# Optimization experiments

Hardware: AMD Instinct MI355X
Metric: run time of the kernel (lower is better)

Reference implementation:

```python
import jax, jax.numpy as jnp
import numpy as np

K = 7          # kernel_size
PAD = 3        # padding (same-size output)
GROUPS = 8


def _unfold(z, H, W):
    # z: [B, C, H+2p, W+2p] -> patches [B, C, H, W, K*K], flat index = kh*K + kw
    # matches torch .unfold(2,K,1).unfold(3,K,1).view(..., -1)
    return jnp.stack(
        [z[:, :, a:a + H, b:b + W] for a in range(K) for b in range(K)],
        axis=-1,
    )


def setup_inputs() -> dict:
    key = jax.random.key(0)
    ks = jax.random.split(key, 7)
    B, C, H, W = 4, 64, 64, 64
    Cout = 64
    fan_scale = (2.0 / Cout) ** 0.5  # kaiming fan_out, 1x1 conv
    return {
        "x": jax.random.normal(ks[0], (B, C, H, W), jnp.float32),
        "y": jax.random.normal(ks[1], (B, C, H, W), jnp.float32),
        "Wq": jax.random.normal(ks[2], (Cout, C), jnp.float32) * fan_scale,
        "Wk": jax.random.normal(ks[3], (Cout, C), jnp.float32) * fan_scale,
        "Wv": jax.random.normal(ks[4], (Cout, C), jnp.float32) * fan_scale,
        "rel_h": jax.random.normal(ks[5], (Cout // 2, K), jnp.float32),
        "rel_w": jax.random.normal(ks[6], (Cout // 2, K), jnp.float32),
    }


def reference(x, y, Wq, Wk, Wv, rel_h, rel_w):
    B, C, H, W = x.shape
    Cout = Wq.shape[0]
    half = Cout // 2

    # 1x1 convs (no bias) commute with zero padding, so project first.
    q = jnp.einsum('oc,bchw->bohw', Wq, x)          # [B, Cout, H, W]
    k_full = jnp.einsum('oc,bchw->bohw', Wk, x)
    v_full = jnp.einsum('oc,bchw->bohw', Wv, y)

    pad4 = ((0, 0), (0, 0), (PAD, PAD), (PAD, PAD))
    k_pat = _unfold(jnp.pad(k_full, pad4), H, W)    # [B, Cout, H, W, K*K]
    v_pat = _unfold(jnp.pad(v_full, pad4), H, W)

    # relative-position bias: rel_h over kh (top half of channels), rel_w over kw
    bias_h = jnp.broadcast_to(rel_h[:, :, None], (half, K, K))   # [Cout/2, kh, kw]
    bias_w = jnp.broadcast_to(rel_w[:, None, :], (half, K, K))
    bias = jnp.concatenate([bias_h, bias_w], axis=0).reshape(Cout, K * K)
    k_pat = k_pat + bias[None, :, None, None, :]

    cg = Cout // GROUPS
    k_pat = k_pat.reshape(B, GROUPS, cg, H, W, K * K)
    v_pat = v_pat.reshape(B, GROUPS, cg, H, W, K * K)
    q = q.reshape(B, GROUPS, cg, H, W, 1)

    attn = jax.nn.softmax(q * k_pat, axis=-1)       # per-channel softmax over window
    out = jnp.sum(attn * v_pat, axis=-1)            # [B, G, cg, H, W]
    return out.reshape(B, Cout, H, W)
```

## Files before the change

### kernel.cpp

```cpp
#include <hip/hip_runtime.h>

#define HW 4096

typedef float f4 __attribute__((ext_vector_type(4)));
typedef float f2 __attribute__((ext_vector_type(2)));

__global__ __launch_bounds__(256) void proj_kernel(
    const float* __restrict__ x, const float* __restrict__ y,
    const float* __restrict__ Wq, const float* __restrict__ Wk,
    const float* __restrict__ Wv,
    float* __restrict__ qkv)
{
    const int sp = blockIdx.x >> 5;
    const int m  = sp >> 3;
    const int r0 = (sp & 7) * 8;
    const int pi = (blockIdx.x & 31) * 256 + threadIdx.x;
    const int px = pi * 2;
    const int b  = px >> 12;
    const int pp = px & 4095;

    const float* W   = (m == 0) ? Wq : (m == 1) ? Wk : Wv;
    const float* src = (m == 2) ? y : x;
    const float* sb  = src + (size_t)b * 64 * HW + pp;

    f2 acc[8];
#pragma unroll
    for (int j = 0; j < 8; ++j) acc[j] = (f2){0.f, 0.f};

#pragma unroll
    for (int cb = 0; cb < 8; ++cb) {
        f2 xv[8];
#pragma unroll
        for (int c2 = 0; c2 < 8; ++c2)
            xv[c2] = *(const f2*)&sb[(cb * 8 + c2) * HW];
#pragma unroll
        for (int j = 0; j < 8; ++j) {
            const float* wr = W + (r0 + j) * 64 + cb * 8;
#pragma unroll
            for (int c2 = 0; c2 < 8; ++c2) {
                acc[j][0] = fmaf(wr[c2], xv[c2][0], acc[j][0]);
                acc[j][1] = fmaf(wr[c2], xv[c2][1], acc[j][1]);
            }
        }
    }

    float* dstm = qkv + ((size_t)m << 20) + (size_t)b * 64 * HW + pp;
#pragma unroll
    for (int j = 0; j < 8; ++j)
        *(f2*)&dstm[(size_t)(r0 + j) * HW] = acc[j];
}

__global__ __launch_bounds__(256) void attn_kernel(
    const float* __restrict__ qg, const float* __restrict__ kg,
    const float* __restrict__ vg,
    const float* __restrict__ rel_h, const float* __restrict__ rel_w,
    float* __restrict__ out)
{
    __shared__ float kT[22 * 72];
    __shared__ float vT[22 * 72];

    const int blk = blockIdx.x;
    const int bc  = blk >> 2;
    const int h0  = (blk & 3) << 4;
    const int c   = bc & 63;
    const int t   = threadIdx.x;

    const float* kimg = kg + (size_t)bc * HW;
    const float* vimg = vg + (size_t)bc * HW;
    const f4 z4 = {0.f, 0.f, 0.f, 0.f};

    if (t < 88) {
        const int row = t >> 2, side = (t >> 1) & 1, arr = t & 1;
        float* dst = arr ? vT : kT;
        *(f4*)&dst[row * 72 + side * 68] = z4;
    }
#pragma unroll
    for (int j = 0; j < 2; ++j) {
        const int idx = j * 256 + t;
        if (idx < 352) {
            const int row = idx >> 4, ch = idx & 15;
            const int hy = h0 - 3 + row;
            const bool rv = ((unsigned)hy < 64u);
            const f4 kv = rv ? *(const f4*)&kimg[hy * 64 + ch * 4] : z4;
            const f4 vv = rv ? *(const f4*)&vimg[hy * 64 + ch * 4] : z4;
            *(f4*)&kT[row * 72 + ch * 4 + 4] = kv;
            *(f4*)&vT[row * 72 + ch * 4 + 4] = vv;
        }
    }
    __syncthreads();

    const int r  = t >> 4;
    const int w0 = (t & 15) << 2;
    const int h  = h0 + r;

    const float LOG2E = 1.4426950408889634f;
    const f4 qv = *(const f4*)&qg[(size_t)bc * HW + h * 64 + w0];
    float qe[4];
#pragma unroll
    for (int p = 0; p < 4; ++p) qe[p] = qv[p] * LOG2E;

    float qb[7][4];
    if (c < 32) {
#pragma unroll
        for (int a = 0; a < 7; ++a) {
            const float bb = rel_h[c * 7 + a];
#pragma unroll
            for (int p = 0; p < 4; ++p) qb[a][p] = qe[p] * bb;
        }
    } else {
#pragma unroll
        for (int j = 0; j < 7; ++j) {
            const float bb = rel_w[(c - 32) * 7 + j];
#pragma unroll
            for (int p = 0; p < 4; ++p) qb[j][p] = qe[p] * bb;
        }
    }

    float l[4] = {0.f, 0.f, 0.f, 0.f};
    float o[4] = {0.f, 0.f, 0.f, 0.f};

    if (c < 32) {
#pragma unroll
        for (int a = 0; a < 7; ++a) {
            const int ro = (r + a) * 72 + w0;
            const f4 k0 = *(const f4*)&kT[ro];
            const f4 k1 = *(const f4*)&kT[ro + 4];
            const f4 k2 = *(const f4*)&kT[ro + 8];
            const f4 v0 = *(const f4*)&vT[ro];
            const f4 v1 = *(const f4*)&vT[ro + 4];
            const f4 v2 = *(const f4*)&vT[ro + 8];
            const float kw[12] = {k0[0], k0[1], k0[2], k0[3], k1[0], k1[1], k1[2], k1[3],
                                  k2[0], k2[1], k2[2], k2[3]};
            const float vw[12] = {v0[0], v0[1], v0[2], v0[3], v1[0], v1[1], v1[2], v1[3],
                                  v2[0], v2[1], v2[2], v2[3]};
#pragma unroll
            for (int b2 = 0; b2 < 7; ++b2)
#pragma unroll
                for (int p = 0; p < 4; ++p) {
                    const float s = fmaf(qe[p], kw[p + b2 + 1], qb[a][p]);
                    const float e = __builtin_amdgcn_exp2f(s);
                    l[p] += e;
                    o[p] = fmaf(e, vw[p + b2 + 1], o[p]);
                }
        }
    } else {
#pragma unroll
        for (int a = 0; a < 7; ++a) {
            const int ro = (r + a) * 72 + w0;
            const f4 k0 = *(const f4*)&kT[ro];
            const f4 k1 = *(const f4*)&kT[ro + 4];
            const f4 k2 = *(const f4*)&kT[ro + 8];
            const f4 v0 = *(const f4*)&vT[ro];
            const f4 v1 = *(const f4*)&vT[ro + 4];
            const f4 v2 = *(const f4*)&vT[ro + 8];
            const float kw[12] = {k0[0], k0[1], k0[2], k0[3], k1[0], k1[1], k1[2], k1[3],
                                  k2[0], k2[1], k2[2], k2[3]};
            const float vw[12] = {v0[0], v0[1], v0[2], v0[3], v1[0], v1[1], v1[2], v1[3],
                                  v2[0], v2[1], v2[2], v2[3]};
#pragma unroll
            for (int b2 = 0; b2 < 7; ++b2)
#pragma unroll
                for (int p = 0; p < 4; ++p) {
                    const float s = fmaf(qe[p], kw[p + b2 + 1], qb[b2][p]);
                    const float e = __builtin_amdgcn_exp2f(s);
                    l[p] += e;
                    o[p] = fmaf(e, vw[p + b2 + 1], o[p]);
                }
        }
    }

    f4 res;
#pragma unroll
    for (int p = 0; p < 4; ++p)
        res[p] = o[p] * __builtin_amdgcn_rcpf(l[p]);
    *(f4*)&out[(size_t)bc * HW + h * 64 + w0] = res;
}

extern "C" void kernel_launch(void* const* d_in, const int* in_sizes, int n_in,
                              void* d_out, int out_size, void* d_ws, size_t ws_size,
                              hipStream_t stream) {
    const float* x   = (const float*)d_in[0];
    const float* y   = (const float*)d_in[1];
    const float* Wq  = (const float*)d_in[2];
    const float* Wk  = (const float*)d_in[3];
    const float* Wv  = (const float*)d_in[4];
    const float* rlh = (const float*)d_in[5];
    const float* rlw = (const float*)d_in[6];
    float* out = (float*)d_out;

    float* qkv = (float*)d_ws;
    float* q = qkv;
    float* k = qkv + (1 << 20);
    float* v = qkv + (2 << 20);

    proj_kernel<<<768, 256, 0, stream>>>(x, y, Wq, Wk, Wv, qkv);
    attn_kernel<<<1024, 256, 0, stream>>>(q, k, v, rlh, rlw, out);
}
```

Baseline: 94.43 us.

## Stage input tile in shared memory and share it across output-row groups in projection

The projection kernel now loads a 64-channel by 128-pixel input tile into LDS once per block, and each of four wavefronts computes 8 output rows from it using a wave-uniform row-group index. Each block covers half of the 64 output channels, so global input reads are reused across 32 output rows instead of re-read by 8 separate row-slices. The inner FMA is also rewritten as a packed two-wide fma so it can use packed FP32 instructions. This adds 32KB of LDS per block and a barrier, which may limit occupancy.

```diff
diff --git a/kernel.cpp b/kernel.cpp
--- a/kernel.cpp
+++ b/kernel.cpp
@@ -11,17 +11,33 @@
     const float* __restrict__ Wv,
     float* __restrict__ qkv)
 {
-    const int sp = blockIdx.x >> 5;
-    const int m  = sp >> 3;
-    const int r0 = (sp & 7) * 8;
-    const int pi = (blockIdx.x & 31) * 256 + threadIdx.x;
-    const int px = pi * 2;
-    const int b  = px >> 12;
-    const int pp = px & 4095;
+    __shared__ float xT[64 * 128];
+
+    const int pb   = blockIdx.x & 127;
+    const int sp   = blockIdx.x >> 7;
+    const int m    = sp >> 1;
+    const int half = sp & 1;
+    const int t    = threadIdx.x;
+
+    const int b   = pb >> 5;
+    const int pp0 = (pb & 31) * 128;
 
     const float* W   = (m == 0) ? Wq : (m == 1) ? Wk : Wv;
     const float* src = (m == 2) ? y : x;
-    const float* sb  = src + (size_t)b * 64 * HW + pp;
+    const float* sb0 = src + (size_t)b * 64 * HW + pp0;
+
+#pragma unroll
+    for (int i = 0; i < 8; ++i) {
+        const int chunk = i * 256 + t;
+        const int c = chunk >> 5;
+        const int o = (chunk & 31) * 4;
+        *(f4*)&xT[c * 128 + o] = *(const f4*)&sb0[c * HW + o];
+    }
+    __syncthreads();
+
+    const int g  = __builtin_amdgcn_readfirstlane(t >> 6);
+    const int p  = t & 63;
+    const int r0 = half * 32 + g * 8;
 
     f2 acc[8];
 #pragma unroll
@@ -29,25 +45,25 @@
 
 #pragma unroll
     for (int cb = 0; cb < 8; ++cb) {
-        f2 xv[8];
+        f2 xs[8];
 #pragma unroll
         for (int c2 = 0; c2 < 8; ++c2)
-            xv[c2] = *(const f2*)&sb[(cb * 8 + c2) * HW];
+            xs[c2] = *(const f2*)&xT[(cb * 8 + c2) * 128 + p * 2];
 #pragma unroll
         for (int j = 0; j < 8; ++j) {
             const float* wr = W + (r0 + j) * 64 + cb * 8;
 #pragma unroll
             for (int c2 = 0; c2 < 8; ++c2) {
-                acc[j][0] = fmaf(wr[c2], xv[c2][0], acc[j][0]);
-                acc[j][1] = fmaf(wr[c2], xv[c2][1], acc[j][1]);
+                const f2 w2 = {wr[c2], wr[c2]};
+                acc[j] = __builtin_elementwise_fma(w2, xs[c2], acc[j]);
             }
         }
     }
 
-    float* dstm = qkv + ((size_t)m << 20) + (size_t)b * 64 * HW + pp;
+    float* dstm = qkv + ((size_t)m << 20) + (size_t)b * 64 * HW + pp0;
 #pragma unroll
     for (int j = 0; j < 8; ++j)
-        *(f2*)&dstm[(size_t)(r0 + j) * HW] = acc[j];
+        *(f2*)&dstm[(size_t)(r0 + j) * HW + p * 2] = acc[j];
 }
 
 __global__ __launch_bounds__(256) void attn_kernel(
```

Result: no change. 93.84 us (-0.6%).
